# Kernel optimization log

Measured on AMD Instinct MI355X. Metric: run time of the kernel, lower is better.

Reference implementation:

```python
import jax, jax.numpy as jnp
import numpy as np

B, C, S = 16, 8, 128
DT, DX, DY = 0.001, 1.0, 1.0
NUM_STEPS = 10
EPS = 1e-6


def _thomas(a, b, c, d):
    """Batched Thomas tridiagonal solve. a,b,c,d: [M,N] rows; solve along N."""
    aT, bT, cT, dT = a.T, b.T, c.T, d.T  # [N, M]
    zero = jnp.zeros_like(dT[0])

    def fwd(carry, inp):
        cs_p, ds_p = carry
        ai, bi, ci, di = inp
        denom = bi - ai * cs_p + EPS  # i=0: cs_p=0 -> denom = b0 + eps (matches torch)
        cs = ci / denom
        ds = (di - ai * ds_p) / denom
        return (cs, ds), (cs, ds)

    _, (c_star, d_star) = jax.lax.scan(fwd, (zero, zero), (aT, bT, cT, dT))

    def bwd(x_next, inp):
        ci, di = inp
        x = di - ci * x_next
        return x, x

    _, xs = jax.lax.scan(bwd, d_star[-1], (c_star[:-1], d_star[:-1]), reverse=True)
    x = jnp.concatenate([xs, d_star[-1:]], axis=0)  # [N, M]
    return x.T


def _diffuse_rows(u2d, coeff):
    """Implicit 1D diffusion along last axis. u2d, coeff: [M,N]."""
    a = -coeff
    c = -coeff
    b = 1.0 + 2.0 * coeff
    b = b.at[:, 0].set(1.0 + coeff[:, 0])
    b = b.at[:, -1].set(1.0 + coeff[:, -1])
    return _thomas(a, b, c, u2d)


def _forward(u, alpha_base, beta_base, alpha_time_coeff, beta_time_coeff, channel_mixing):
    Bb, Cc, H, W = u.shape
    half = DT / 2.0
    t = 0.0
    for _ in range(NUM_STEPS):
        # x half-step (coefficient alpha at time t)
        alpha = jnp.clip(alpha_base + alpha_time_coeff * t, EPS, 10.0)
        u = jnp.einsum('dc,bchw->bdhw', channel_mixing, u)
        uf = u.reshape(Bb * Cc, H, W)
        af = jnp.broadcast_to(alpha[None], (Bb, Cc, H, W)).reshape(Bb * Cc, H, W)
        uf = _diffuse_rows(uf.reshape(-1, W), af.reshape(-1, W) * half / DX**2).reshape(Bb * Cc, H, W)
        t += half
        # y full step (coefficient beta at time t+dt/2)
        beta = jnp.clip(beta_base + beta_time_coeff * t, EPS, 10.0)
        bf = jnp.broadcast_to(beta[None], (Bb, Cc, H, W)).reshape(Bb * Cc, H, W)
        ut = uf.transpose(0, 2, 1).reshape(-1, H)
        bt = bf.transpose(0, 2, 1).reshape(-1, H)
        ut = _diffuse_rows(ut, bt * DT / DY**2)
        uf = ut.reshape(Bb * Cc, W, H).transpose(0, 2, 1)
        t += half
        # x half-step (coefficient alpha at time t+dt)
        alpha = jnp.clip(alpha_base + alpha_time_coeff * t, EPS, 10.0)
        af = jnp.broadcast_to(alpha[None], (Bb, Cc, H, W)).reshape(Bb * Cc, H, W)
        uf = _diffuse_rows(uf.reshape(-1, W), af.reshape(-1, W) * half / DX**2).reshape(Bb * Cc, H, W)
        u = uf.reshape(Bb, Cc, H, W)
    return u


def setup_inputs() -> dict:
    key = jax.random.key(0)
    k_u, k_cm, k_atc, k_btc = jax.random.split(key, 4)
    u = jax.random.normal(k_u, (B, C, S, S), dtype=jnp.float32)
    alpha_base = jnp.ones((C, S, S), dtype=jnp.float32)
    beta_base = jnp.ones((C, S, S), dtype=jnp.float32)
    alpha_time_coeff = jax.random.normal(k_atc, (C, S, S), dtype=jnp.float32) * 0.01
    beta_time_coeff = jax.random.normal(k_btc, (C, S, S), dtype=jnp.float32) * 0.01
    channel_mixing = jnp.eye(C, dtype=jnp.float32) + jax.random.normal(k_cm, (C, C), dtype=jnp.float32) * 0.01
    return {
        'u': u,
        'alpha_base': alpha_base,
        'beta_base': beta_base,
        'alpha_time_coeff': alpha_time_coeff,
        'beta_time_coeff': beta_time_coeff,
        'channel_mixing': channel_mixing,
    }


def reference(u, alpha_base, beta_base, alpha_time_coeff, beta_time_coeff, channel_mixing):
    return _forward(u, alpha_base, beta_base, alpha_time_coeff, beta_time_coeff, channel_mixing)
```

## Files before the change

kernel.cpp:

```cpp
#include <hip/hip_runtime.h>


constexpr int S_ = 128;
constexpr int RS = 129;
constexpr float EPSF = 1e-6f;

constexpr int OFF_A = 0;
constexpr int OFF_B = 12384;
constexpr int OFF_C = 24768;
constexpr int POOL  = 33024;

__device__ __forceinline__ void jrun(const float (&e)[12], const float (&g)[12],
                                     float (&o)[8]) {
    float x1[12];
    #pragma unroll
    for (int i = 1; i <= 10; ++i) x1[i] = fmaf(g[i], e[i - 1] + e[i + 1], e[i]);
    #pragma unroll
    for (int i = 2; i <= 9; ++i) o[i - 2] = fmaf(g[i], x1[i - 1] + x1[i + 1], e[i]);
}

template <bool HEAD, bool TAILMIX>
__global__ __launch_bounds__(512, 2) void step_kernel(
    const float* __restrict__ usrc, float* __restrict__ udst,
    const float* __restrict__ ab, const float* __restrict__ atc,
    const float* __restrict__ bbeta, const float* __restrict__ btc,
    const float* __restrict__ cm, float t_y, float t_x)
{
    __shared__ float sP[POOL];
    const int tid = threadIdx.x;
    const int b   = blockIdx.x >> 4;
    const int h0  = (blockIdx.x & 15) << 3;

    if (HEAD) {
        #pragma unroll
        for (int m = 0; m < 2; ++m) {
            const int col = tid + 512 * m;
            const int c = col >> 7, w = col & 127;
            #pragma unroll
            for (int hh = 0; hh < 12; ++hh) {
                const int gh = h0 - 2 + hh;
                float v = 0.f;
                if (gh >= 0 && gh < S_) v = usrc[((b * 8 + c) * S_ + gh) * S_ + w];
                sP[OFF_A + (c * 12 + hh) * RS + w] = v;
            }
        }
        __syncthreads();
        {
            float M[64];
            #pragma unroll
            for (int i = 0; i < 64; ++i) M[i] = cm[i];
            #pragma unroll
            for (int m = 0; m < 3; ++m) {
                const int p = tid + 512 * m;
                const int hh = p >> 7, w = p & 127;
                float v[8], o[8];
                #pragma unroll
                for (int c = 0; c < 8; ++c) v[c] = sP[OFF_A + (c * 12 + hh) * RS + w];
                #pragma unroll
                for (int dd = 0; dd < 8; ++dd) {
                    float a = 0.f;
                    #pragma unroll
                    for (int c = 0; c < 8; ++c) a = fmaf(M[dd * 8 + c], v[c], a);
                    o[dd] = a;
                }
                #pragma unroll
                for (int c = 0; c < 8; ++c) sP[OFF_A + (c * 12 + hh) * RS + w] = o[c];
            }
        }
        __syncthreads();
        #pragma unroll
        for (int m = 0; m < 3; ++m) {
            const int run = tid + 512 * m;
            const int r96 = run % 96;
            const int wr  = run / 96;
            const int c = r96 / 12, hh = r96 % 12;
            const int gh = h0 - 2 + hh;
            const int w0 = wr * 8;
            const bool rowin = (gh >= 0 && gh < S_);
            float e[12], g[12];
            #pragma unroll
            for (int j = 0; j < 12; ++j) {
                const int wj = w0 - 2 + j;
                const bool win = (wj >= 0 && wj < S_);
                const float dv = win ? sP[OFF_A + r96 * RS + wj] : 0.f;
                float co = 0.f;
                if (rowin && win) {
                    float al = ab[(c * S_ + gh) * S_ + wj];
                    al = fminf(fmaxf(al, EPSF), 10.f);
                    co = al * 0.0005f;
                }
                const float nb = (wj == 0 || wj == S_ - 1) ? 1.f : 2.f;
                const float rb = __builtin_amdgcn_rcpf(fmaf(nb, co, 1.f) + EPSF);
                e[j] = rb * dv; g[j] = rb * co;
            }
            float o[8]; jrun(e, g, o);
            #pragma unroll
            for (int i = 0; i < 8; ++i) sP[OFF_B + r96 * RS + w0 + i] = o[i];
        }
        __syncthreads();
    }

    #pragma unroll
    for (int m = 0; m < 2; ++m) {
        const int col = tid + 512 * m;
        const int c = col >> 7, w = col & 127;
        float e[12], g[12];
        #pragma unroll
        for (int hh = 0; hh < 12; ++hh) {
            const int gh = h0 - 2 + hh;
            const bool inr = (gh >= 0 && gh < S_);
            const int ghc = inr ? gh : 0;
            float dv;
            if (HEAD) dv = sP[OFF_B + (c * 12 + hh) * RS + w];
            else      dv = inr ? usrc[((b * 8 + c) * S_ + ghc) * S_ + w] : 0.f;
            const int gc = (c * S_ + ghc) * S_ + w;
            float be = fmaf(btc[gc], t_y, bbeta[gc]);
            be = fminf(fmaxf(be, EPSF), 10.f);
            const float co = inr ? be * 0.001f : 0.f;
            const float nb = (gh == 0 || gh == S_ - 1) ? 1.f : 2.f;
            const float rb = __builtin_amdgcn_rcpf(fmaf(nb, co, 1.f) + EPSF);
            e[hh] = rb * dv; g[hh] = rb * co;
        }
        float o[8]; jrun(e, g, o);
        #pragma unroll
        for (int i = 0; i < 8; ++i) sP[OFF_A + (c * 8 + i) * RS + w] = o[i];
    }
    #pragma unroll
    for (int m = 0; m < 16; ++m) {
        const int p = tid + 512 * m;
        const int r = p >> 7, w = p & 127;
        const int c = r >> 3, ho = r & 7;
        const int gc = (c * S_ + h0 + ho) * S_ + w;
        float al = fmaf(atc[gc], t_x, ab[gc]);
        al = fminf(fmaxf(al, EPSF), 10.f);
        sP[OFF_C + r * RS + w] = al * 0.0005f;
    }
    __syncthreads();

    float rbk[2][12], gk[2][12], xo[2][8];
    #pragma unroll
    for (int m = 0; m < 2; ++m) {
        const int run = tid + 512 * m;
        const int r = run & 63, wr = run >> 6;
        const int w0 = wr * 8;
        float e[12];
        #pragma unroll
        for (int j = 0; j < 12; ++j) {
            const int wj = w0 - 2 + j;
            const bool win = (wj >= 0 && wj < S_);
            const float co = win ? sP[OFF_C + r * RS + wj] : 0.f;
            const float dv = win ? sP[OFF_A + r * RS + wj] : 0.f;
            const float nb = (wj == 0 || wj == S_ - 1) ? 1.f : 2.f;
            const float rb = __builtin_amdgcn_rcpf(fmaf(nb, co, 1.f) + EPSF);
            rbk[m][j] = rb; gk[m][j] = rb * co;
            e[j] = rb * dv;
        }
        jrun(e, gk[m], xo[m]);
    }

    if (TAILMIX) {
        #pragma unroll
        for (int m = 0; m < 2; ++m) {
            const int run = tid + 512 * m;
            const int r = run & 63, w0 = (run >> 6) * 8;
            #pragma unroll
            for (int i = 0; i < 8; ++i) sP[OFF_B + r * RS + w0 + i] = xo[m][i];
        }
        __syncthreads();
        float M[64];
        #pragma unroll
        for (int i = 0; i < 64; ++i) M[i] = cm[i];
        #pragma unroll
        for (int m = 0; m < 2; ++m) {
            const int p = tid + 512 * m;
            const int ho = p >> 7, w = p & 127;
            float v[8], o[8];
            #pragma unroll
            for (int c = 0; c < 8; ++c) v[c] = sP[OFF_B + (c * 8 + ho) * RS + w];
            #pragma unroll
            for (int dd = 0; dd < 8; ++dd) {
                float a = 0.f;
                #pragma unroll
                for (int c = 0; c < 8; ++c) a = fmaf(M[dd * 8 + c], v[c], a);
                o[dd] = a;
            }
            #pragma unroll
            for (int c = 0; c < 8; ++c) sP[OFF_A + (c * 8 + ho) * RS + w] = o[c];
        }
        __syncthreads();
        #pragma unroll
        for (int m = 0; m < 2; ++m) {
            const int run = tid + 512 * m;
            const int r = run & 63, wr = run >> 6;
            const int w0 = wr * 8;
            const int c = r >> 3, ho = r & 7;
            float e[12];
            #pragma unroll
            for (int j = 0; j < 12; ++j) {
                const int wj = w0 - 2 + j;
                const bool win = (wj >= 0 && wj < S_);
                const float dv = win ? sP[OFF_A + r * RS + wj] : 0.f;
                e[j] = rbk[m][j] * dv;
            }
            float o[8]; jrun(e, gk[m], o);
            float4* dst4 = (float4*)&udst[((b * 8 + c) * S_ + h0 + ho) * S_ + w0];
            dst4[0] = make_float4(o[0], o[1], o[2], o[3]);
            dst4[1] = make_float4(o[4], o[5], o[6], o[7]);
        }
    } else {
        #pragma unroll
        for (int m = 0; m < 2; ++m) {
            const int run = tid + 512 * m;
            const int r = run & 63, wr = run >> 6;
            const int w0 = wr * 8;
            const int c = r >> 3, ho = r & 7;
            float4* dst4 = (float4*)&udst[((b * 8 + c) * S_ + h0 + ho) * S_ + w0];
            dst4[0] = make_float4(xo[m][0], xo[m][1], xo[m][2], xo[m][3]);
            dst4[1] = make_float4(xo[m][4], xo[m][5], xo[m][6], xo[m][7]);
        }
    }
}

extern "C" void kernel_launch(void* const* d_in, const int* in_sizes, int n_in,
                              void* d_out, int out_size, void* d_ws, size_t ws_size,
                              hipStream_t stream) {
    const float* u_in = (const float*)d_in[0];
    const float* ab   = (const float*)d_in[1];
    const float* bbta = (const float*)d_in[2];
    const float* atc  = (const float*)d_in[3];
    const float* btc  = (const float*)d_in[4];
    const float* cm   = (const float*)d_in[5];
    float* uo = (float*)d_out;
    float* uw = (float*)d_ws;

    const dim3 g(256), blk(512);
    const float dt2 = 0.0005f;

    step_kernel<true, true><<<g, blk, 0, stream>>>(u_in, uw, ab, atc, bbta, btc, cm,
                                                   1 * dt2, 2 * dt2);
    const float* src = uw; float* dst = uo;
    for (int k = 1; k <= 8; ++k) {
        step_kernel<false, true><<<g, blk, 0, stream>>>(src, dst, ab, atc, bbta, btc, cm,
                                                        (2 * k + 1) * dt2, (2 * k + 2) * dt2);
        const float* ns = dst; dst = (dst == uo) ? uw : uo; src = ns;
    }
    step_kernel<false, false><<<g, blk, 0, stream>>>(src, dst, ab, atc, bbta, btc, cm,
                                                     19 * dt2, 20 * dt2);
}
```

Measured before the change: 179.3 us.

## Precompute fp16 diffusion coefficients and store intermediate state in fp16

```diff
diff --git a/kernel.cpp b/kernel.cpp
--- a/kernel.cpp
+++ b/kernel.cpp
@@ -1,37 +1,74 @@
 #include <hip/hip_runtime.h>
-
-
-constexpr int S_ = 128;
-constexpr int RS = 129;
+#include <hip/hip_fp16.h>
+
+
+constexpr int S_  = 128;
+constexpr int RS  = 129;
 constexpr float EPSF = 1e-6f;
-
-constexpr int OFF_A = 0;
-constexpr int OFF_B = 12384;
-constexpr int OFF_C = 24768;
-constexpr int POOL  = 33024;
-
-__device__ __forceinline__ void jrun(const float (&e)[12], const float (&g)[12],
-                                     float (&o)[8]) {
-    float x1[12];
-    #pragma unroll
-    for (int i = 1; i <= 10; ++i) x1[i] = fmaf(g[i], e[i - 1] + e[i + 1], e[i]);
-    #pragma unroll
-    for (int i = 2; i <= 9; ++i) o[i - 2] = fmaf(g[i], x1[i - 1] + x1[i + 1], e[i]);
-}
-
-template <bool HEAD, bool TAILMIX>
+constexpr int CSS = 8 * 128 * 128;
+
+__device__ __forceinline__ float2 decf(uint cb) {
+    __half2 h = *reinterpret_cast<__half2*>(&cb);
+    return __half22float2(h);
+}
+
+template <int N>
+__device__ __forceinline__ void jrunN(const float (&e)[N], const float (&g)[N],
+                                      float (&o)[N - 4]) {
+    float x1[N];
+    #pragma unroll
+    for (int i = 1; i <= N - 2; ++i) x1[i] = fmaf(g[i], e[i - 1] + e[i + 1], e[i]);
+    #pragma unroll
+    for (int i = 2; i <= N - 3; ++i) o[i - 2] = fmaf(g[i], x1[i - 1] + x1[i + 1], e[i]);
+}
+
+__global__ __launch_bounds__(256) void coef_kernel(
+    const float* __restrict__ ab, const float* __restrict__ atc,
+    const float* __restrict__ bb, const float* __restrict__ btc,
+    __half2* __restrict__ cf)
+{
+    for (int gc = blockIdx.x * 256 + threadIdx.x; gc < CSS; gc += gridDim.x * 256) {
+        const int w = gc & 127, h = (gc >> 7) & 127;
+        const float abv = ab[gc], atv = atc[gc], bbv = bb[gc], btv = btc[gc];
+        const float nbY = (h == 0 || h == S_ - 1) ? 1.f : 2.f;
+        const float nbX = (w == 0 || w == S_ - 1) ? 1.f : 2.f;
+        for (int k = 0; k < 10; ++k) {
+            const float ty = (2 * k + 1) * 0.0005f;
+            const float tx = (2 * k + 2) * 0.0005f;
+            float be = fminf(fmaxf(fmaf(btv, ty, bbv), EPSF), 10.f);
+            float co = be * 0.001f;
+            float rb = __builtin_amdgcn_rcpf(fmaf(nbY, co, 1.f) + EPSF);
+            cf[k * CSS + gc] = __floats2half2_rn(rb * co, rb - 1.f);
+            float al = fminf(fmaxf(fmaf(atv, tx, abv), EPSF), 10.f);
+            co = al * 0.0005f;
+            rb = __builtin_amdgcn_rcpf(fmaf(nbX, co, 1.f) + EPSF);
+            cf[(10 + k) * CSS + gc] = __floats2half2_rn(rb * co, rb - 1.f);
+        }
+        float al = fminf(fmaxf(abv, EPSF), 10.f);
+        float co = al * 0.0005f;
+        float rb = __builtin_amdgcn_rcpf(fmaf(nbX, co, 1.f) + EPSF);
+        cf[20 * CSS + gc] = __floats2half2_rn(rb * co, rb - 1.f);
+    }
+}
+
+template <bool HEAD, bool LASTK>
 __global__ __launch_bounds__(512, 2) void step_kernel(
-    const float* __restrict__ usrc, float* __restrict__ udst,
-    const float* __restrict__ ab, const float* __restrict__ atc,
-    const float* __restrict__ bbeta, const float* __restrict__ btc,
-    const float* __restrict__ cm, float t_y, float t_x)
+    const void* __restrict__ usrc_, void* __restrict__ udst_,
+    const __half2* __restrict__ cfy, const __half2* __restrict__ cfx,
+    const __half2* __restrict__ cfx0, const float* __restrict__ cm)
 {
+    constexpr int POOL   = HEAD ? 288 * RS : 192 * RS;
+    constexpr int OFF_A  = 0;
+    constexpr int OFF_B  = 64 * RS;
+    constexpr int OFF_CP = HEAD ? 192 * RS : 128 * RS;
+    constexpr int OFF_X0 = 96 * RS;
     __shared__ float sP[POOL];
     const int tid = threadIdx.x;
     const int b   = blockIdx.x >> 4;
     const int h0  = (blockIdx.x & 15) << 3;
 
     if (HEAD) {
+        const float* u0 = (const float*)usrc_;
         #pragma unroll
         for (int m = 0; m < 2; ++m) {
             const int col = tid + 512 * m;
@@ -40,9 +77,19 @@
             for (int hh = 0; hh < 12; ++hh) {
                 const int gh = h0 - 2 + hh;
                 float v = 0.f;
-                if (gh >= 0 && gh < S_) v = usrc[((b * 8 + c) * S_ + gh) * S_ + w];
-                sP[OFF_A + (c * 12 + hh) * RS + w] = v;
-            }
+                if (gh >= 0 && gh < S_) v = u0[((b * 8 + c) * S_ + gh) * S_ + w];
+                sP[(c * 12 + hh) * RS + w] = v;
+            }
+        }
+        #pragma unroll
+        for (int m = 0; m < 12; ++m) {
+            const int task = tid + 512 * m;
+            const int r = task >> 6, col2 = task & 63;
+            const int c = r / 12, hh = r % 12;
+            int gh = h0 - 2 + hh; gh = gh < 0 ? 0 : (gh >= S_ ? S_ - 1 : gh);
+            const uint2 v = ((const uint2*)cfx0)[(c * S_ + gh) * 64 + col2];
+            sP[OFF_CP + r * RS + col2 * 2]     = __uint_as_float(v.x);
+            sP[OFF_CP + r * RS + col2 * 2 + 1] = __uint_as_float(v.y);
         }
         __syncthreads();
         {
@@ -55,7 +102,7 @@
                 const int hh = p >> 7, w = p & 127;
                 float v[8], o[8];
                 #pragma unroll
-                for (int c = 0; c < 8; ++c) v[c] = sP[OFF_A + (c * 12 + hh) * RS + w];
+                for (int c = 0; c < 8; ++c) v[c] = sP[(c * 12 + hh) * RS + w];
                 #pragma unroll
                 for (int dd = 0; dd < 8; ++dd) {
                     float a = 0.f;
@@ -64,42 +111,38 @@
                     o[dd] = a;
                 }
                 #pragma unroll
-                for (int c = 0; c < 8; ++c) sP[OFF_A + (c * 12 + hh) * RS + w] = o[c];
+                for (int c = 0; c < 8; ++c) sP[(c * 12 + hh) * RS + w] = o[c];
             }
         }
         __syncthreads();
         #pragma unroll
         for (int m = 0; m < 3; ++m) {
-            const int run = tid + 512 * m;
-            const int r96 = run % 96;
-            const int wr  = run / 96;
+            const int task = tid + 512 * m;
+            const int r96 = task % 96, wr = task / 96;
             const int c = r96 / 12, hh = r96 % 12;
             const int gh = h0 - 2 + hh;
+            const bool rowin = (gh >= 0 && gh < S_);
             const int w0 = wr * 8;
-            const bool rowin = (gh >= 0 && gh < S_);
             float e[12], g[12];
             #pragma unroll
             for (int j = 0; j < 12; ++j) {
                 const int wj = w0 - 2 + j;
                 const bool win = (wj >= 0 && wj < S_);
-                const float dv = win ? sP[OFF_A + r96 * RS + wj] : 0.f;
-                float co = 0.f;
-                if (rowin && win) {
-                    float al = ab[(c * S_ + gh) * S_ + wj];
-                    al = fminf(fmaxf(al, EPSF), 10.f);
-                    co = al * 0.0005f;
-                }
-                const float nb = (wj == 0 || wj == S_ - 1) ? 1.f : 2.f;
-                const float rb = __builtin_amdgcn_rcpf(fmaf(nb, co, 1.f) + EPSF);
-                e[j] = rb * dv; g[j] = rb * co;
-            }
-            float o[8]; jrun(e, g, o);
-            #pragma unroll
-            for (int i = 0; i < 8; ++i) sP[OFF_B + r96 * RS + w0 + i] = o[i];
-        }
-        __syncthreads();
-    }
-
+                const float dv = win ? sP[r96 * RS + wj] : 0.f;
+                const uint cb = (rowin && win)
+                    ? __float_as_uint(sP[OFF_CP + r96 * RS + wj]) : 0u;
+                const float2 f = decf(cb);
+                e[j] = (1.f + f.y) * dv;
+                g[j] = f.x;
+            }
+            float o[8]; jrunN<12>(e, g, o);
+            #pragma unroll
+            for (int i = 0; i < 8; ++i) sP[OFF_X0 + r96 * RS + w0 + i] = o[i];
+        }
+        __syncthreads();
+    }
+
+    const __half* us = (const __half*)usrc_;
     #pragma unroll
     for (int m = 0; m < 2; ++m) {
         const int col = tid + 512 * m;
@@ -111,29 +154,25 @@
             const bool inr = (gh >= 0 && gh < S_);
             const int ghc = inr ? gh : 0;
             float dv;
-            if (HEAD) dv = sP[OFF_B + (c * 12 + hh) * RS + w];
-            else      dv = inr ? usrc[((b * 8 + c) * S_ + ghc) * S_ + w] : 0.f;
-            const int gc = (c * S_ + ghc) * S_ + w;
-            float be = fmaf(btc[gc], t_y, bbeta[gc]);
-            be = fminf(fmaxf(be, EPSF), 10.f);
-            const float co = inr ? be * 0.001f : 0.f;
-            const float nb = (gh == 0 || gh == S_ - 1) ? 1.f : 2.f;
-            const float rb = __builtin_amdgcn_rcpf(fmaf(nb, co, 1.f) + EPSF);
-            e[hh] = rb * dv; g[hh] = rb * co;
-        }
-        float o[8]; jrun(e, g, o);
+            if (HEAD) dv = sP[OFF_X0 + (c * 12 + hh) * RS + w];
+            else      dv = inr ? __half2float(us[((b * 8 + c) * S_ + ghc) * S_ + w]) : 0.f;
+            const __half2 cy = cfy[(c * S_ + ghc) * S_ + w];
+            const float2 f = __half22float2(cy);
+            e[hh] = (1.f + f.y) * dv;
+            g[hh] = inr ? f.x : 0.f;
+        }
+        float o[8]; jrunN<12>(e, g, o);
         #pragma unroll
         for (int i = 0; i < 8; ++i) sP[OFF_A + (c * 8 + i) * RS + w] = o[i];
     }
     #pragma unroll
-    for (int m = 0; m < 16; ++m) {
-        const int p = tid + 512 * m;
-        const int r = p >> 7, w = p & 127;
+    for (int m = 0; m < 8; ++m) {
+        const int task = tid + 512 * m;
+        const int r = task >> 6, col2 = task & 63;
         const int c = r >> 3, ho = r & 7;
-        const int gc = (c * S_ + h0 + ho) * S_ + w;
-        float al = fmaf(atc[gc], t_x, ab[gc]);
-        al = fminf(fmaxf(al, EPSF), 10.f);
-        sP[OFF_C + r * RS + w] = al * 0.0005f;
+        const uint2 v = ((const uint2*)cfx)[(c * S_ + h0 + ho) * 64 + col2];
+        sP[OFF_CP + r * RS + col2 * 2]     = __uint_as_float(v.x);
+        sP[OFF_CP + r * RS + col2 * 2 + 1] = __uint_as_float(v.y);
     }
     __syncthreads();
 
@@ -148,17 +187,27 @@
         for (int j = 0; j < 12; ++j) {
             const int wj = w0 - 2 + j;
             const bool win = (wj >= 0 && wj < S_);
-            const float co = win ? sP[OFF_C + r * RS + wj] : 0.f;
             const float dv = win ? sP[OFF_A + r * RS + wj] : 0.f;
-            const float nb = (wj == 0 || wj == S_ - 1) ? 1.f : 2.f;
-            const float rb = __builtin_amdgcn_rcpf(fmaf(nb, co, 1.f) + EPSF);
-            rbk[m][j] = rb; gk[m][j] = rb * co;
-            e[j] = rb * dv;
-        }
-        jrun(e, gk[m], xo[m]);
-    }
-
-    if (TAILMIX) {
+            const uint cb = win ? __float_as_uint(sP[OFF_CP + r * RS + wj]) : 0u;
+            const float2 f = decf(cb);
+            rbk[m][j] = 1.f + f.y; gk[m][j] = f.x;
+            e[j] = rbk[m][j] * dv;
+        }
+        jrunN<12>(e, gk[m], xo[m]);
+    }
+
+    if (LASTK) {
+        float* ud = (float*)udst_;
+        #pragma unroll
+        for (int m = 0; m < 2; ++m) {
+            const int run = tid + 512 * m;
+            const int r = run & 63, wr = run >> 6;
+            const int c = r >> 3, ho = r & 7;
+            float4* dst4 = (float4*)&ud[((b * 8 + c) * S_ + h0 + ho) * S_ + wr * 8];
+            dst4[0] = make_float4(xo[m][0], xo[m][1], xo[m][2], xo[m][3]);
+            dst4[1] = make_float4(xo[m][4], xo[m][5], xo[m][6], xo[m][7]);
+        }
+    } else {
         #pragma unroll
         for (int m = 0; m < 2; ++m) {
             const int run = tid + 512 * m;
@@ -188,6 +237,7 @@
             for (int c = 0; c < 8; ++c) sP[OFF_A + (c * 8 + ho) * RS + w] = o[c];
         }
         __syncthreads();
+        __half* ud = (__half*)udst_;
         #pragma unroll
         for (int m = 0; m < 2; ++m) {
             const int run = tid + 512 * m;
@@ -202,21 +252,12 @@
                 const float dv = win ? sP[OFF_A + r * RS + wj] : 0.f;
                 e[j] = rbk[m][j] * dv;
             }
-            float o[8]; jrun(e, gk[m], o);
-            float4* dst4 = (float4*)&udst[((b * 8 + c) * S_ + h0 + ho) * S_ + w0];
-            dst4[0] = make_float4(o[0], o[1], o[2], o[3]);
-            dst4[1] = make_float4(o[4], o[5], o[6], o[7]);
-        }
-    } else {
-        #pragma unroll
-        for (int m = 0; m < 2; ++m) {
-            const int run = tid + 512 * m;
-            const int r = run & 63, wr = run >> 6;
-            const int w0 = wr * 8;
-            const int c = r >> 3, ho = r & 7;
-            float4* dst4 = (float4*)&udst[((b * 8 + c) * S_ + h0 + ho) * S_ + w0];
-            dst4[0] = make_float4(xo[m][0], xo[m][1], xo[m][2], xo[m][3]);
-            dst4[1] = make_float4(xo[m][4], xo[m][5], xo[m][6], xo[m][7]);
+            float o[8]; jrunN<12>(e, gk[m], o);
+            __half2* d2 = (__half2*)&ud[((b * 8 + c) * S_ + h0 + ho) * S_ + w0];
+            d2[0] = __floats2half2_rn(o[0], o[1]);
+            d2[1] = __floats2half2_rn(o[2], o[3]);
+            d2[2] = __floats2half2_rn(o[4], o[5]);
+            d2[3] = __floats2half2_rn(o[6], o[7]);
         }
     }
 }
@@ -231,19 +272,23 @@
     const float* btc  = (const float*)d_in[4];
     const float* cm   = (const float*)d_in[5];
     float* uo = (float*)d_out;
-    float* uw = (float*)d_ws;
+    __half*  h1 = (__half*)d_ws;
+    __half*  h2 = (__half*)((char*)d_ws + (8u << 20));
+    __half2* cf = (__half2*)((char*)d_ws + (16u << 20));
+
+    coef_kernel<<<dim3(512), dim3(256), 0, stream>>>(ab, atc, bbta, btc, cf);
 
     const dim3 g(256), blk(512);
-    const float dt2 = 0.0005f;
-
-    step_kernel<true, true><<<g, blk, 0, stream>>>(u_in, uw, ab, atc, bbta, btc, cm,
-                                                   1 * dt2, 2 * dt2);
-    const float* src = uw; float* dst = uo;
+    step_kernel<true, false><<<g, blk, 0, stream>>>(u_in, h1, cf + 0 * CSS,
+                                                    cf + 10 * CSS, cf + 20 * CSS, cm);
+    const __half* s = h1; __half* d = h2;
     for (int k = 1; k <= 8; ++k) {
-        step_kernel<false, true><<<g, blk, 0, stream>>>(src, dst, ab, atc, bbta, btc, cm,
-                                                        (2 * k + 1) * dt2, (2 * k + 2) * dt2);
-        const float* ns = dst; dst = (dst == uo) ? uw : uo; src = ns;
-    }
-    step_kernel<false, false><<<g, blk, 0, stream>>>(src, dst, ab, atc, bbta, btc, cm,
-                                                     19 * dt2, 20 * dt2);
-}
+        step_kernel<false, false><<<g, blk, 0, stream>>>(s, d, cf + k * CSS,
+                                                         cf + (10 + k) * CSS, cf, cm);
+        const __half* ns = d;
+        d = (d == h2) ? h1 : h2;
+        s = ns;
+    }
+    step_kernel<false, true><<<g, blk, 0, stream>>>(s, uo, cf + 9 * CSS,
+                                                    cf + 19 * CSS, cf, cm);
+}
```

Result: faster. 166.5 us (-7.2%).
